# Kernel tuning notes

Hardware: AMD Instinct MI355X
Metric: run time of the kernel (lower is better)

The kernel has to match this reference:

```python
import jax, jax.numpy as jnp
import numpy as np

B, G, T, D = 512, 10, 100, 50
H, EMB, NEMB, OUT = 30, 20, 10, 10


def _gru_last_hidden(x, W_ih, W_hh, b_ih, b_hh):
    """PyTorch-convention GRU over x:[N,T,D]; returns final hidden [N,H].
    Gate order in the 3H dim is (r, z, n), matching torch.nn.GRU."""
    N = x.shape[0]
    # precompute input projections for all timesteps: [N,T,3H] -> [T,N,3H]
    xw = jnp.einsum('ntd,gd->ntg', x, W_ih) + b_ih
    xw = jnp.swapaxes(xw, 0, 1)
    h0 = jnp.zeros((N, H), dtype=x.dtype)

    def step(h, xw_t):
        gh = h @ W_hh.T + b_hh                      # [N,3H]
        r = jax.nn.sigmoid(xw_t[:, :H] + gh[:, :H])
        z = jax.nn.sigmoid(xw_t[:, H:2 * H] + gh[:, H:2 * H])
        n = jnp.tanh(xw_t[:, 2 * H:] + r * gh[:, 2 * H:])
        h = (1.0 - z) * n + z * h
        return h, None

    hT, _ = jax.lax.scan(step, h0, xw)
    return hT


def setup_inputs() -> dict:
    key = jax.random.key(0)
    ks = jax.random.split(key, 12)
    s_g = 1.0 / np.sqrt(H)
    inp = {
        'input1': jax.random.normal(ks[0], (B, G, T, D), jnp.float32),
        'input2': jax.random.normal(ks[1], (B, G, T, D), jnp.float32),
        'W_ih': jax.random.normal(ks[2], (3 * H, D), jnp.float32) * s_g,
        'W_hh': jax.random.normal(ks[3], (3 * H, H), jnp.float32) * s_g,
        'b_ih': jax.random.normal(ks[4], (3 * H,), jnp.float32) * s_g,
        'b_hh': jax.random.normal(ks[5], (3 * H,), jnp.float32) * s_g,
        'W1': jax.random.normal(ks[6], (EMB, H * G), jnp.float32) / np.sqrt(H * G),
        'b1': jax.random.normal(ks[7], (EMB,), jnp.float32) * 0.01,
        'W2': jax.random.normal(ks[8], (NEMB, EMB), jnp.float32) / np.sqrt(EMB),
        'b2': jax.random.normal(ks[9], (NEMB,), jnp.float32) * 0.01,
        'W3': jax.random.normal(ks[10], (OUT, NEMB), jnp.float32) / np.sqrt(NEMB),
        'b3': jax.random.normal(ks[11], (OUT,), jnp.float32) * 0.01,
    }
    return inp


def reference(input1, input2, W_ih, W_hh, b_ih, b_hh, W1, b1, W2, b2, W3, b3):
    gelu = lambda v: jax.nn.gelu(v, approximate=False)  # torch GELU default = exact
    # Fuse all num_gru slices of both inputs into one big batched GRU call
    x = jnp.concatenate([input1, input2], axis=0).reshape(2 * B * G, T, D)
    hT = _gru_last_hidden(x, W_ih, W_hh, b_ih, b_hh)    # [2BG, H]
    h = hT.reshape(2, B, G * H)                          # cat over num_gru == reshape
    embeddings1, embeddings2 = h[0], h[1]               # random_dis, MLP input
    logit_emb = gelu(embeddings2 @ W1.T + b1) @ W2.T + b2
    logit = gelu(logit_emb) @ W3.T + b3
    return logit, embeddings1
```

## Files before the change

### kernel.cpp

```cpp
#include <hip/hip_runtime.h>
#include <hip/hip_bf16.h>
#include <math.h>

#define T_    100
#define D_    50
#define H_    30
#define HALF  5120
#define EMB_  20
#define NEMB_ 10
#define OUT_  10

typedef _Float16 h2    __attribute__((ext_vector_type(2)));
typedef _Float16 f16x8 __attribute__((ext_vector_type(8)));
typedef float    f32x4 __attribute__((ext_vector_type(4)));

union FR  { f16x8 v; h2 p[4]; float4 f4; };

__device__ __forceinline__ h2 pk(float a, float b) {
    return __builtin_bit_cast(h2, __builtin_amdgcn_cvt_pkrtz(a, b));
}
__device__ __forceinline__ int pki(float a, float b) {
    return __builtin_bit_cast(int, __builtin_amdgcn_cvt_pkrtz(a, b));
}

#if __has_builtin(__builtin_amdgcn_exp2f)
#define EXP2(x) __builtin_amdgcn_exp2f(x)
#else
#define EXP2(x) exp2f(x)
#endif

struct XR { float2 a0, a1, a2, a3, b0, b1, b2, b3; };

__device__ __forceinline__ int rho(int j) {
    return (j & 3) + 4 * (j >> 3) + 16 * ((j >> 2) & 1);
}

__global__ __launch_bounds__(64, 1) void gru_kernel(
    const float* __restrict__ input1, const float* __restrict__ input2,
    const float* __restrict__ W_ih,  const float* __restrict__ W_hh,
    const float* __restrict__ b_ih,  const float* __restrict__ b_hh,
    float* __restrict__ emb1_out,
    float* __restrict__ h2_out)
{
    const int lane = threadIdx.x & 63;
    const int s    = lane & 15;
    const int q    = lane >> 4;
    const int n    = blockIdx.x * 16 + s;

    __shared__ __align__(16) _Float16 Wst [96 * 64];
    __shared__ __align__(16) _Float16 Whst[96 * 32];

    const float SC_RZ = -1.4426950408889634f;
    const float SC_N  =  2.8853900817779268f;

    for (int i = lane; i < 1536; i += 64) ((unsigned long long*)Wst)[i]  = 0ull;
    for (int i = lane; i < 768;  i += 64) ((unsigned long long*)Whst)[i] = 0ull;

    for (int i = 0; i < 71; ++i) {
        int idx = lane + i * 64;
        if (idx < 4500) {
            int rw = idx / 50, k = idx - rw * 50;
            int g  = rw / 30,  j = rw - g * 30;
            int ge = g * 32 + rho(j);
            float sc = (g < 2) ? SC_RZ : SC_N;
            Wst[ge * 64 + k] = (_Float16)(W_ih[idx] * sc);
        }
    }
    for (int i = 0; i < 2; ++i) {
        int idx = lane + i * 64;
        if (idx < 90) {
            int g = idx / 30, j = idx - g * 30;
            int ge = g * 32 + rho(j);
            float sc = (g < 2) ? SC_RZ : SC_N;
            Wst[ge * 64 + 50] = (_Float16)(b_ih[idx] * sc);
        }
    }
    for (int i = 0; i < 43; ++i) {
        int idx = lane + i * 64;
        if (idx < 2700) {
            int rw = idx / 30, k = idx - rw * 30;
            int g  = rw / 30,  j = rw - g * 30;
            int ge = g * 32 + rho(j);
            float sc = (g < 2) ? SC_RZ : SC_N;
            Whst[ge * 32 + k] = (_Float16)(W_hh[idx] * sc);
        }
    }
    for (int i = 0; i < 2; ++i) {
        int idx = lane + i * 64;
        if (idx < 90) {
            int g = idx / 30, j = idx - g * 30;
            int ge = g * 32 + rho(j);
            float sc = (g < 2) ? SC_RZ : SC_N;
            Whst[ge * 32 + 30] = (_Float16)(b_hh[idx] * sc);
        }
    }
    __syncthreads();

    FR wih[6][2], whh[6];
    #pragma unroll
    for (int nt = 0; nt < 6; ++nt) {
        wih[nt][0].f4 = *(const float4*)&Wst [(nt * 16 + s) * 64 + q * 8];
        wih[nt][1].f4 = *(const float4*)&Wst [(nt * 16 + s) * 64 + 32 + q * 8];
        whh[nt].f4    = *(const float4*)&Whst[(nt * 16 + s) * 32 + q * 8];
    }

    const float* xp = (n < HALF) ? input1 + (size_t)n * (T_ * D_)
                                 : input2 + (size_t)(n - HALF) * (T_ * D_);

    auto load_x = [&](int t, XR& X) {
        const float* r  = xp + t * D_;
        const float* pa = r + q * 8;
        const float* pb = (q < 2) ? (r + 32 + q * 8) : r;
        const float* p0 = (q == 2) ? (r + 48) : pb;
        X.a0 = *(const float2*)(pa + 0);
        X.a1 = *(const float2*)(pa + 2);
        X.a2 = *(const float2*)(pa + 4);
        X.a3 = *(const float2*)(pa + 6);
        X.b0 = *(const float2*)(p0);
        X.b1 = *(const float2*)(pb + 2);
        X.b2 = *(const float2*)(pb + 4);
        X.b3 = *(const float2*)(pb + 6);
    };
    auto build = [&](const XR& X, FR& x0, FR& x1) {
        x0.p[0] = pk(X.a0.x, X.a0.y); x0.p[1] = pk(X.a1.x, X.a1.y);
        x0.p[2] = pk(X.a2.x, X.a2.y); x0.p[3] = pk(X.a3.x, X.a3.y);
        if (q < 2) {
            x1.p[0] = pk(X.b0.x, X.b0.y); x1.p[1] = pk(X.b1.x, X.b1.y);
            x1.p[2] = pk(X.b2.x, X.b2.y); x1.p[3] = pk(X.b3.x, X.b3.y);
        } else if (q == 2) {
            x1.p[0] = pk(X.b0.x, X.b0.y); x1.p[1] = pk(1.f, 0.f);
            x1.p[2] = pk(0.f, 0.f);       x1.p[3] = pk(0.f, 0.f);
        } else {
            x1.p[0] = pk(0.f, 0.f); x1.p[1] = pk(0.f, 0.f);
            x1.p[2] = pk(0.f, 0.f); x1.p[3] = pk(0.f, 0.f);
        }
    };

    float hold[8] = {0.f, 0.f, 0.f, 0.f, 0.f, 0.f, 0.f, 0.f};
    int w0 = 0, w1 = 0, w2 = 0, w3 = 0;
    const int ONE = pki(1.f, 0.f);

    auto xphase = [&](XR& X, int tload, f32x4 (&xacc)[6]) {
        FR x0, x1;
        build(X, x0, x1);
        load_x(tload, X);
        #pragma unroll
        for (int i = 0; i < 6; ++i) {
            f32x4 zz = {0.f, 0.f, 0.f, 0.f};
            f32x4 a = __builtin_amdgcn_mfma_f32_16x16x32_f16(wih[i][0].v, x0.v, zz, 0, 0, 0);
            xacc[i] = __builtin_amdgcn_mfma_f32_16x16x32_f16(wih[i][1].v, x1.v, a, 0, 0, 0);
        }
    };
    auto step_h = [&](const f32x4 (&xacc)[6], f32x4 (&arz)[4], f32x4 (&ah)[2]) {
        FR bh;
        bh.p[0] = __builtin_bit_cast(h2, w0);
        bh.p[1] = __builtin_bit_cast(h2, w1);
        bh.p[2] = __builtin_bit_cast(h2, w2);
        bh.p[3] = __builtin_bit_cast(h2, q == 3 ? ONE : w3);
        #pragma unroll
        for (int nt = 0; nt < 4; ++nt)
            arz[nt] = __builtin_amdgcn_mfma_f32_16x16x32_f16(whh[nt].v, bh.v, xacc[nt], 0, 0, 0);
        #pragma unroll
        for (int u = 0; u < 2; ++u) {
            f32x4 zz = {0.f, 0.f, 0.f, 0.f};
            ah[u] = __builtin_amdgcn_mfma_f32_16x16x32_f16(whh[4 + u].v, bh.v, zz, 0, 0, 0);
        }
    };
    auto step_fin = [&](const f32x4 (&arz)[4], const f32x4 (&ah)[2],
                        const f32x4 (&xacc)[6]) {
        #pragma unroll
        for (int u = 0; u < 2; ++u) {
            #pragma unroll
            for (int r = 0; r < 4; ++r) {
                const float er = EXP2(arz[u][r]);
                const float rg = __builtin_amdgcn_rcpf(1.f + er);
                const float ez = EXP2(arz[2 + u][r]);
                const float aa = fmaf(rg, ah[u][r], xacc[4 + u][r]);
                const float et = EXP2(aa);
                const float oz = 1.f + ez, ot = 1.f + et;
                const float ip = __builtin_amdgcn_rcpf(oz * ot);
                const float zg = ot * ip;
                const float th = fmaf(-2.f * oz, ip, 1.f);
                hold[u * 4 + r] = fmaf(zg, hold[u * 4 + r] - th, th);
            }
        }
        w0 = pki(hold[0], hold[1]); w1 = pki(hold[2], hold[3]);
        w2 = pki(hold[4], hold[5]); w3 = pki(hold[6], hold[7]);
    };

    XR X0, X1, X2, X3;
    load_x(0, X0); load_x(1, X1); load_x(2, X2); load_x(3, X3);
    f32x4 xaccA[6], xaccB[6];
    {
        FR x0, x1;
        build(X0, x0, x1);
        load_x(4, X0);
        #pragma unroll
        for (int i = 0; i < 6; ++i) {
            f32x4 zz = {0.f, 0.f, 0.f, 0.f};
            f32x4 a = __builtin_amdgcn_mfma_f32_16x16x32_f16(wih[i][0].v, x0.v, zz, 0, 0, 0);
            xaccA[i] = __builtin_amdgcn_mfma_f32_16x16x32_f16(wih[i][1].v, x1.v, a, 0, 0, 0);
        }
    }

    #pragma unroll 1
    for (int k = 0; k < 25; ++k) {
        const int t = 4 * k;
        f32x4 arz[4], ah[2];
        step_h(xaccA, arz, ah);
        xphase(X1, (t + 5 < 100 ? t + 5 : 99), xaccB);
        step_fin(arz, ah, xaccA);
        step_h(xaccB, arz, ah);
        xphase(X2, (t + 6 < 100 ? t + 6 : 99), xaccA);
        step_fin(arz, ah, xaccB);
        step_h(xaccA, arz, ah);
        xphase(X3, (t + 7 < 100 ? t + 7 : 99), xaccB);
        step_fin(arz, ah, xaccA);
        step_h(xaccB, arz, ah);
        xphase(X0, (t + 8 < 100 ? t + 8 : 99), xaccA);
        step_fin(arz, ah, xaccB);
    }

    float* outp = (n < HALF) ? emb1_out + (size_t)n * H_
                             : h2_out + (size_t)(n - HALF) * H_;
    #pragma unroll
    for (int u = 0; u < 2; ++u)
        #pragma unroll
        for (int r = 0; r < 4; ++r) {
            const int j = 8 * q + 4 * u + r;
            if (j < H_) outp[j] = hold[u * 4 + r];
        }
}

__global__ __launch_bounds__(64) void mlp_kernel(
    const float* __restrict__ h2i,
    const float* __restrict__ W1, const float* __restrict__ b1,
    const float* __restrict__ W2, const float* __restrict__ b2,
    const float* __restrict__ W3, const float* __restrict__ b3,
    float* __restrict__ logit)
{
    const int b    = blockIdx.x;
    const int lane = threadIdx.x;
    __shared__ float e2[300];
    const float* row = h2i + (size_t)b * 300;
    #pragma unroll
    for (int i = lane; i < 75; i += 64)
        *(float4*)&e2[i * 4] = *(const float4*)(row + i * 4);
    __syncthreads();

    const float kInvSqrt2 = 0.70710678118654752f;
    float y1 = 0.f;
    if (lane < EMB_) {
        float acc = b1[lane];
        const float* wp = W1 + lane * 300;
        #pragma unroll
        for (int qq = 0; qq < 75; ++qq) {
            float4 wv = *(const float4*)(wp + qq * 4);
            acc += wv.x * e2[qq*4 + 0] + wv.y * e2[qq*4 + 1]
                 + wv.z * e2[qq*4 + 2] + wv.w * e2[qq*4 + 3];
        }
        y1 = 0.5f * acc * (1.f + erff(acc * kInvSqrt2));
    }
    float acc2 = (lane < NEMB_) ? b2[lane] : 0.f;
    #pragma unroll
    for (int e = 0; e < EMB_; ++e) {
        const float v = __shfl(y1, e);
        if (lane < NEMB_) acc2 += v * W2[lane * EMB_ + e];
    }
    const float y2 = 0.5f * acc2 * (1.f + erff(acc2 * kInvSqrt2));
    float acc3 = (lane < OUT_) ? b3[lane] : 0.f;
    #pragma unroll
    for (int e = 0; e < NEMB_; ++e) {
        const float v = __shfl(y2, e);
        if (lane < OUT_) acc3 += v * W3[lane * NEMB_ + e];
    }
    if (lane < OUT_) logit[(size_t)b * OUT_ + lane] = acc3;
}

extern "C" void kernel_launch(void* const* d_in, const int* in_sizes, int n_in,
                              void* d_out, int out_size, void* d_ws, size_t ws_size,
                              hipStream_t stream) {
    const float* input1 = (const float*)d_in[0];
    const float* input2 = (const float*)d_in[1];
    const float* W_ih   = (const float*)d_in[2];
    const float* W_hh   = (const float*)d_in[3];
    const float* b_ih   = (const float*)d_in[4];
    const float* b_hh   = (const float*)d_in[5];
    const float* W1     = (const float*)d_in[6];
    const float* b1     = (const float*)d_in[7];
    const float* W2     = (const float*)d_in[8];
    const float* b2     = (const float*)d_in[9];
    const float* W3     = (const float*)d_in[10];
    const float* b3     = (const float*)d_in[11];

    float* out = (float*)d_out;
    float* h2s = (float*)d_ws;

    hipLaunchKernelGGL(gru_kernel, dim3(640), dim3(64), 0, stream,
                       input1, input2, W_ih, W_hh, b_ih, b_hh,
                       out + 5120, h2s);
    hipLaunchKernelGGL(mlp_kernel, dim3(512), dim3(64), 0, stream,
                       h2s, W1, b1, W2, b2, W3, b3, out);
}
```

Measured before the change: 101.8 us.

## Stage GRU input chunks through double-buffered LDS with coalesced float4 loads

Replaces the per-lane strided float2 global loads of x with cooperative coalesced float4 loads of four-timestep chunks for all 16 sequences into a double-buffered shared-memory tile. Each step then reads its MFMA operands from LDS, and the next chunk's global load is issued one chunk ahead. The aim is better global coalescing and more latency hiding. In exchange it adds about 27KB of LDS and 13 float4 registers per lane, and there is no explicit barrier between the LDS write and the read. That is only safe because the block is a single wavefront.

```diff
diff --git a/kernel.cpp b/kernel.cpp
--- a/kernel.cpp
+++ b/kernel.cpp
@@ -49,6 +49,7 @@
 
     __shared__ __align__(16) _Float16 Wst [96 * 64];
     __shared__ __align__(16) _Float16 Whst[96 * 32];
+    __shared__ __align__(16) float    Xb[2][16 * 212];
 
     const float SC_RZ = -1.4426950408889634f;
     const float SC_N  =  2.8853900817779268f;
@@ -104,11 +105,34 @@
         whh[nt].f4    = *(const float4*)&Whst[(nt * 16 + s) * 32 + q * 8];
     }
 
-    const float* xp = (n < HALF) ? input1 + (size_t)n * (T_ * D_)
-                                 : input2 + (size_t)(n - HALF) * (T_ * D_);
-
-    auto load_x = [&](int t, XR& X) {
-        const float* r  = xp + t * D_;
+    const int n0 = blockIdx.x * 16;
+    const float* srcbase = (n0 < HALF) ? input1 + (size_t)n0 * (T_ * D_)
+                                       : input2 + (size_t)(n0 - HALF) * (T_ * D_);
+
+    int Poff[13], Wf[13];
+    #pragma unroll
+    for (int i = 0; i < 13; ++i) {
+        int g   = lane + i * 64;
+        int gg  = (g < 800) ? g : 0;
+        int sq  = gg / 50, rem = gg - sq * 50;
+        Poff[i] = sq * (T_ * D_) + rem * 4;
+        Wf[i]   = sq * 212 + rem * 4;
+    }
+    float4 G[13];
+    auto stage_load = [&](int cc) {
+        #pragma unroll
+        for (int i = 0; i < 13; ++i)
+            G[i] = *(const float4*)(srcbase + Poff[i] + cc * 200);
+    };
+    auto stage_write = [&](int nb) {
+        #pragma unroll
+        for (int i = 0; i < 13; ++i)
+            if (i < 12 || lane < 32)
+                *(float4*)&Xb[nb][Wf[i]] = G[i];
+    };
+
+    auto lds_read_x = [&](int buf, int tt, XR& X) {
+        const float* r  = &Xb[buf][s * 212 + tt * 50];
         const float* pa = r + q * 8;
         const float* pb = (q < 2) ? (r + 32 + q * 8) : r;
         const float* p0 = (q == 2) ? (r + 48) : pb;
@@ -140,10 +164,10 @@
     int w0 = 0, w1 = 0, w2 = 0, w3 = 0;
     const int ONE = pki(1.f, 0.f);
 
-    auto xphase = [&](XR& X, int tload, f32x4 (&xacc)[6]) {
-        FR x0, x1;
+    auto xphase = [&](int buf, int tt, f32x4 (&xacc)[6]) {
+        FR x0, x1; XR X;
+        lds_read_x(buf, tt, X);
         build(X, x0, x1);
-        load_x(tload, X);
         #pragma unroll
         for (int i = 0; i < 6; ++i) {
             f32x4 zz = {0.f, 0.f, 0.f, 0.f};
@@ -188,37 +212,22 @@
         w2 = pki(hold[4], hold[5]); w3 = pki(hold[6], hold[7]);
     };
 
-    XR X0, X1, X2, X3;
-    load_x(0, X0); load_x(1, X1); load_x(2, X2); load_x(3, X3);
+    stage_load(0);
+    stage_write(0);
+    stage_load(1);
     f32x4 xaccA[6], xaccB[6];
-    {
-        FR x0, x1;
-        build(X0, x0, x1);
-        load_x(4, X0);
-        #pragma unroll
-        for (int i = 0; i < 6; ++i) {
-            f32x4 zz = {0.f, 0.f, 0.f, 0.f};
-            f32x4 a = __builtin_amdgcn_mfma_f32_16x16x32_f16(wih[i][0].v, x0.v, zz, 0, 0, 0);
-            xaccA[i] = __builtin_amdgcn_mfma_f32_16x16x32_f16(wih[i][1].v, x1.v, a, 0, 0, 0);
-        }
-    }
+    xphase(0, 0, xaccA);
 
     #pragma unroll 1
-    for (int k = 0; k < 25; ++k) {
-        const int t = 4 * k;
+    for (int c = 0; c < 25; ++c) {
+        const int cur = c & 1, nxt = cur ^ 1;
+        stage_write(nxt);
+        stage_load(c + 2 > 24 ? 24 : c + 2);
         f32x4 arz[4], ah[2];
-        step_h(xaccA, arz, ah);
-        xphase(X1, (t + 5 < 100 ? t + 5 : 99), xaccB);
-        step_fin(arz, ah, xaccA);
-        step_h(xaccB, arz, ah);
-        xphase(X2, (t + 6 < 100 ? t + 6 : 99), xaccA);
-        step_fin(arz, ah, xaccB);
-        step_h(xaccA, arz, ah);
-        xphase(X3, (t + 7 < 100 ? t + 7 : 99), xaccB);
-        step_fin(arz, ah, xaccA);
-        step_h(xaccB, arz, ah);
-        xphase(X0, (t + 8 < 100 ? t + 8 : 99), xaccA);
-        step_fin(arz, ah, xaccB);
+        step_h(xaccA, arz, ah); xphase(cur, 1, xaccB); step_fin(arz, ah, xaccA);
+        step_h(xaccB, arz, ah); xphase(cur, 2, xaccA); step_fin(arz, ah, xaccB);
+        step_h(xaccA, arz, ah); xphase(cur, 3, xaccB); step_fin(arz, ah, xaccA);
+        step_h(xaccB, arz, ah); xphase(nxt, 0, xaccA); step_fin(arz, ah, xaccB);
     }
 
     float* outp = (n < HALF) ? emb1_out + (size_t)n * H_
```

After: 155.6 us. 1.53x slower.

## Split GRU hidden units across two wavefronts with LDS hidden-state exchange

Applied to the files above, without the earlier changes.

Each block now runs two wavefronts, and each wave owns half of the hidden units (one 16-row tile per gate). This halves the per-wave MFMA and transcendental work on the serial recurrence chain. The hidden state is exchanged through double-buffered shared memory with a barrier every timestep. In exchange it adds per-step LDS round trips and barrier latency on the critical path, while the x loads are duplicated in both waves.

```diff
diff --git a/kernel.cpp b/kernel.cpp
--- a/kernel.cpp
+++ b/kernel.cpp
@@ -35,29 +35,33 @@
     return (j & 3) + 4 * (j >> 3) + 16 * ((j >> 2) & 1);
 }
 
-__global__ __launch_bounds__(64, 1) void gru_kernel(
+__global__ __launch_bounds__(128, 1) void gru_kernel(
     const float* __restrict__ input1, const float* __restrict__ input2,
     const float* __restrict__ W_ih,  const float* __restrict__ W_hh,
     const float* __restrict__ b_ih,  const float* __restrict__ b_hh,
     float* __restrict__ emb1_out,
     float* __restrict__ h2_out)
 {
-    const int lane = threadIdx.x & 63;
+    const int tid  = threadIdx.x;
+    const int lane = tid & 63;
+    const int wv   = tid >> 6;
     const int s    = lane & 15;
     const int q    = lane >> 4;
     const int n    = blockIdx.x * 16 + s;
 
     __shared__ __align__(16) _Float16 Wst [96 * 64];
     __shared__ __align__(16) _Float16 Whst[96 * 32];
+    __shared__ __align__(8)  int2     Hx[2][2][64];
 
     const float SC_RZ = -1.4426950408889634f;
     const float SC_N  =  2.8853900817779268f;
 
-    for (int i = lane; i < 1536; i += 64) ((unsigned long long*)Wst)[i]  = 0ull;
-    for (int i = lane; i < 768;  i += 64) ((unsigned long long*)Whst)[i] = 0ull;
-
-    for (int i = 0; i < 71; ++i) {
-        int idx = lane + i * 64;
+    for (int i = tid; i < 1536; i += 128) ((unsigned long long*)Wst)[i]  = 0ull;
+    for (int i = tid; i < 768;  i += 128) ((unsigned long long*)Whst)[i] = 0ull;
+    __syncthreads();
+
+    for (int i = 0; i < 36; ++i) {
+        int idx = tid + i * 128;
         if (idx < 4500) {
             int rw = idx / 50, k = idx - rw * 50;
             int g  = rw / 30,  j = rw - g * 30;
@@ -66,17 +70,14 @@
             Wst[ge * 64 + k] = (_Float16)(W_ih[idx] * sc);
         }
     }
-    for (int i = 0; i < 2; ++i) {
-        int idx = lane + i * 64;
-        if (idx < 90) {
-            int g = idx / 30, j = idx - g * 30;
-            int ge = g * 32 + rho(j);
-            float sc = (g < 2) ? SC_RZ : SC_N;
-            Wst[ge * 64 + 50] = (_Float16)(b_ih[idx] * sc);
-        }
-    }
-    for (int i = 0; i < 43; ++i) {
-        int idx = lane + i * 64;
+    if (tid < 90) {
+        int g = tid / 30, j = tid - g * 30;
+        int ge = g * 32 + rho(j);
+        float sc = (g < 2) ? SC_RZ : SC_N;
+        Wst[ge * 64 + 50] = (_Float16)(b_ih[tid] * sc);
+    }
+    for (int i = 0; i < 22; ++i) {
+        int idx = tid + i * 128;
         if (idx < 2700) {
             int rw = idx / 30, k = idx - rw * 30;
             int g  = rw / 30,  j = rw - g * 30;
@@ -85,24 +86,25 @@
             Whst[ge * 32 + k] = (_Float16)(W_hh[idx] * sc);
         }
     }
-    for (int i = 0; i < 2; ++i) {
-        int idx = lane + i * 64;
-        if (idx < 90) {
-            int g = idx / 30, j = idx - g * 30;
-            int ge = g * 32 + rho(j);
-            float sc = (g < 2) ? SC_RZ : SC_N;
-            Whst[ge * 32 + 30] = (_Float16)(b_hh[idx] * sc);
-        }
+    if (tid < 90) {
+        int g = tid / 30, j = tid - g * 30;
+        int ge = g * 32 + rho(j);
+        float sc = (g < 2) ? SC_RZ : SC_N;
+        Whst[ge * 32 + 30] = (_Float16)(b_hh[tid] * sc);
     }
     __syncthreads();
 
-    FR wih[6][2], whh[6];
-    #pragma unroll
-    for (int nt = 0; nt < 6; ++nt) {
-        wih[nt][0].f4 = *(const float4*)&Wst [(nt * 16 + s) * 64 + q * 8];
-        wih[nt][1].f4 = *(const float4*)&Wst [(nt * 16 + s) * 64 + 32 + q * 8];
-        whh[nt].f4    = *(const float4*)&Whst[(nt * 16 + s) * 32 + q * 8];
-    }
+    const int tR = wv, tZ = 2 + wv, tN = 4 + wv;
+    FR wihR0, wihR1, wihZ0, wihZ1, wihN0, wihN1, whhR, whhZ, whhN;
+    wihR0.f4 = *(const float4*)&Wst [(tR * 16 + s) * 64 + q * 8];
+    wihR1.f4 = *(const float4*)&Wst [(tR * 16 + s) * 64 + 32 + q * 8];
+    wihZ0.f4 = *(const float4*)&Wst [(tZ * 16 + s) * 64 + q * 8];
+    wihZ1.f4 = *(const float4*)&Wst [(tZ * 16 + s) * 64 + 32 + q * 8];
+    wihN0.f4 = *(const float4*)&Wst [(tN * 16 + s) * 64 + q * 8];
+    wihN1.f4 = *(const float4*)&Wst [(tN * 16 + s) * 64 + 32 + q * 8];
+    whhR.f4  = *(const float4*)&Whst[(tR * 16 + s) * 32 + q * 8];
+    whhZ.f4  = *(const float4*)&Whst[(tZ * 16 + s) * 32 + q * 8];
+    whhN.f4  = *(const float4*)&Whst[(tN * 16 + s) * 32 + q * 8];
 
     const float* xp = (n < HALF) ? input1 + (size_t)n * (T_ * D_)
                                  : input2 + (size_t)(n - HALF) * (T_ * D_);
@@ -136,100 +138,112 @@
         }
     };
 
-    float hold[8] = {0.f, 0.f, 0.f, 0.f, 0.f, 0.f, 0.f, 0.f};
-    int w0 = 0, w1 = 0, w2 = 0, w3 = 0;
-    const int ONE = pki(1.f, 0.f);
-
-    auto xphase = [&](XR& X, int tload, f32x4 (&xacc)[6]) {
+    float hold[4] = {0.f, 0.f, 0.f, 0.f};
+    int2 mine   = {0, 0};
+    int2 theirs = {0, 0};
+    const int ONE  = pki(1.f, 0.f);
+    const int hidx = s * 4 + q;
+
+    auto xphase = [&](XR& X, int tload, f32x4 (&xacc)[3]) {
         FR x0, x1;
         build(X, x0, x1);
         load_x(tload, X);
+        f32x4 zz = {0.f, 0.f, 0.f, 0.f};
+        f32x4 a;
+        a = __builtin_amdgcn_mfma_f32_16x16x32_f16(wihR0.v, x0.v, zz, 0, 0, 0);
+        xacc[0] = __builtin_amdgcn_mfma_f32_16x16x32_f16(wihR1.v, x1.v, a, 0, 0, 0);
+        a = __builtin_amdgcn_mfma_f32_16x16x32_f16(wihZ0.v, x0.v, zz, 0, 0, 0);
+        xacc[1] = __builtin_amdgcn_mfma_f32_16x16x32_f16(wihZ1.v, x1.v, a, 0, 0, 0);
+        a = __builtin_amdgcn_mfma_f32_16x16x32_f16(wihN0.v, x0.v, zz, 0, 0, 0);
+        xacc[2] = __builtin_amdgcn_mfma_f32_16x16x32_f16(wihN1.v, x1.v, a, 0, 0, 0);
+    };
+    auto step_h = [&](const f32x4 (&xacc)[3], f32x4& ar, f32x4& az, f32x4& anh) {
+        const int p0 = wv ? theirs.x : mine.x;
+        const int p1 = wv ? theirs.y : mine.y;
+        const int p2 = wv ? mine.x   : theirs.x;
+        const int p3 = wv ? mine.y   : theirs.y;
+        FR bh;
+        bh.p[0] = __builtin_bit_cast(h2, p0);
+        bh.p[1] = __builtin_bit_cast(h2, p1);
+        bh.p[2] = __builtin_bit_cast(h2, p2);
+        bh.p[3] = __builtin_bit_cast(h2, q == 3 ? ONE : p3);
+        f32x4 zz = {0.f, 0.f, 0.f, 0.f};
+        ar  = __builtin_amdgcn_mfma_f32_16x16x32_f16(whhR.v, bh.v, xacc[0], 0, 0, 0);
+        az  = __builtin_amdgcn_mfma_f32_16x16x32_f16(whhZ.v, bh.v, xacc[1], 0, 0, 0);
+        anh = __builtin_amdgcn_mfma_f32_16x16x32_f16(whhN.v, bh.v, zz,      0, 0, 0);
+    };
+    auto step_fin = [&](const f32x4& ar, const f32x4& az, const f32x4& anh,
+                        const f32x4& anx) {
         #pragma unroll
-        for (int i = 0; i < 6; ++i) {
-            f32x4 zz = {0.f, 0.f, 0.f, 0.f};
-            f32x4 a = __builtin_amdgcn_mfma_f32_16x16x32_f16(wih[i][0].v, x0.v, zz, 0, 0, 0);
-            xacc[i] = __builtin_amdgcn_mfma_f32_16x16x32_f16(wih[i][1].v, x1.v, a, 0, 0, 0);
-        }
-    };
-    auto step_h = [&](const f32x4 (&xacc)[6], f32x4 (&arz)[4], f32x4 (&ah)[2]) {
-        FR bh;
-        bh.p[0] = __builtin_bit_cast(h2, w0);
-        bh.p[1] = __builtin_bit_cast(h2, w1);
-        bh.p[2] = __builtin_bit_cast(h2, w2);
-        bh.p[3] = __builtin_bit_cast(h2, q == 3 ? ONE : w3);
-        #pragma unroll
-        for (int nt = 0; nt < 4; ++nt)
-            arz[nt] = __builtin_amdgcn_mfma_f32_16x16x32_f16(whh[nt].v, bh.v, xacc[nt], 0, 0, 0);
-        #pragma unroll
-        for (int u = 0; u < 2; ++u) {
-            f32x4 zz = {0.f, 0.f, 0.f, 0.f};
-            ah[u] = __builtin_amdgcn_mfma_f32_16x16x32_f16(whh[4 + u].v, bh.v, zz, 0, 0, 0);
-        }
-    };
-    auto step_fin = [&](const f32x4 (&arz)[4], const f32x4 (&ah)[2],
-                        const f32x4 (&xacc)[6]) {
-        #pragma unroll
-        for (int u = 0; u < 2; ++u) {
-            #pragma unroll
-            for (int r = 0; r < 4; ++r) {
-                const float er = EXP2(arz[u][r]);
-                const float rg = __builtin_amdgcn_rcpf(1.f + er);
-                const float ez = EXP2(arz[2 + u][r]);
-                const float aa = fmaf(rg, ah[u][r], xacc[4 + u][r]);
-                const float et = EXP2(aa);
-                const float oz = 1.f + ez, ot = 1.f + et;
-                const float ip = __builtin_amdgcn_rcpf(oz * ot);
-                const float zg = ot * ip;
-                const float th = fmaf(-2.f * oz, ip, 1.f);
-                hold[u * 4 + r] = fmaf(zg, hold[u * 4 + r] - th, th);
-            }
-        }
-        w0 = pki(hold[0], hold[1]); w1 = pki(hold[2], hold[3]);
-        w2 = pki(hold[4], hold[5]); w3 = pki(hold[6], hold[7]);
+        for (int r = 0; r < 4; ++r) {
+            const float er = EXP2(ar[r]);
+            const float rg = __builtin_amdgcn_rcpf(1.f + er);
+            const float ez = EXP2(az[r]);
+            const float aa = fmaf(rg, anh[r], anx[r]);
+            const float et = EXP2(aa);
+            const float oz = 1.f + ez, ot = 1.f + et;
+            const float ip = __builtin_amdgcn_rcpf(oz * ot);
+            const float zg = ot * ip;
+            const float th = fmaf(-2.f * oz, ip, 1.f);
+            hold[r] = fmaf(zg, hold[r] - th, th);
+        }
+        mine.x = pki(hold[0], hold[1]);
+        mine.y = pki(hold[2], hold[3]);
+    };
+    auto exchange = [&](int par) {
+        Hx[par][wv][hidx] = mine;
+        asm volatile("s_waitcnt lgkmcnt(0)" ::: "memory");
+        __builtin_amdgcn_s_barrier();
+        __builtin_amdgcn_sched_barrier(0);
+        theirs = Hx[par][wv ^ 1][hidx];
     };
 
     XR X0, X1, X2, X3;
     load_x(0, X0); load_x(1, X1); load_x(2, X2); load_x(3, X3);
-    f32x4 xaccA[6], xaccB[6];
+    f32x4 xaccA[3], xaccB[3];
     {
         FR x0, x1;
         build(X0, x0, x1);
         load_x(4, X0);
-        #pragma unroll
-        for (int i = 0; i < 6; ++i) {
-            f32x4 zz = {0.f, 0.f, 0.f, 0.f};
-            f32x4 a = __builtin_amdgcn_mfma_f32_16x16x32_f16(wih[i][0].v, x0.v, zz, 0, 0, 0);
-            xaccA[i] = __builtin_amdgcn_mfma_f32_16x16x32_f16(wih[i][1].v, x1.v, a, 0, 0, 0);
-        }
+        f32x4 zz = {0.f, 0.f, 0.f, 0.f};
+        f32x4 a;
+        a = __builtin_amdgcn_mfma_f32_16x16x32_f16(wihR0.v, x0.v, zz, 0, 0, 0);
+        xaccA[0] = __builtin_amdgcn_mfma_f32_16x16x32_f16(wihR1.v, x1.v, a, 0, 0, 0);
+        a = __builtin_amdgcn_mfma_f32_16x16x32_f16(wihZ0.v, x0.v, zz, 0, 0, 0);
+        xaccA[1] = __builtin_amdgcn_mfma_f32_16x16x32_f16(wihZ1.v, x1.v, a, 0, 0, 0);
+        a = __builtin_amdgcn_mfma_f32_16x16x32_f16(wihN0.v, x0.v, zz, 0, 0, 0);
+        xaccA[2] = __builtin_amdgcn_mfma_f32_16x16x32_f16(wihN1.v, x1.v, a, 0, 0, 0);
     }
 
     #pragma unroll 1
     for (int k = 0; k < 25; ++k) {
         const int t = 4 * k;
-        f32x4 arz[4], ah[2];
-        step_h(xaccA, arz, ah);
+        f32x4 ar, az, anh;
+        step_h(xaccA, ar, az, anh);
         xphase(X1, (t + 5 < 100 ? t + 5 : 99), xaccB);
-        step_fin(arz, ah, xaccA);
-        step_h(xaccB, arz, ah);
+        step_fin(ar, az, anh, xaccA[2]);
+        exchange(0);
+        step_h(xaccB, ar, az, anh);
         xphase(X2, (t + 6 < 100 ? t + 6 : 99), xaccA);
-        step_fin(arz, ah, xaccB);
-        step_h(xaccA, arz, ah);
+        step_fin(ar, az, anh, xaccB[2]);
+        exchange(1);
+        step_h(xaccA, ar, az, anh);
         xphase(X3, (t + 7 < 100 ? t + 7 : 99), xaccB);
-        step_fin(arz, ah, xaccA);
-        step_h(xaccB, arz, ah);
+        step_fin(ar, az, anh, xaccA[2]);
+        exchange(0);
+        step_h(xaccB, ar, az, anh);
         xphase(X0, (t + 8 < 100 ? t + 8 : 99), xaccA);
-        step_fin(arz, ah, xaccB);
+        step_fin(ar, az, anh, xaccB[2]);
+        exchange(1);
     }
 
     float* outp = (n < HALF) ? emb1_out + (size_t)n * H_
                              : h2_out + (size_t)(n - HALF) * H_;
     #pragma unroll
-    for (int u = 0; u < 2; ++u)
-        #pragma unroll
-        for (int r = 0; r < 4; ++r) {
-            const int j = 8 * q + 4 * u + r;
-            if (j < H_) outp[j] = hold[u * 4 + r];
-        }
+    for (int r = 0; r < 4; ++r) {
+        const int j = 8 * q + 4 * wv + r;
+        if (j < H_) outp[j] = hold[r];
+    }
 }
 
 __global__ __launch_bounds__(64) void mlp_kernel(
@@ -296,7 +310,7 @@
     float* out = (float*)d_out;
     float* h2s = (float*)d_ws;
 
-    hipLaunchKernelGGL(gru_kernel, dim3(640), dim3(64), 0, stream,
+    hipLaunchKernelGGL(gru_kernel, dim3(640), dim3(128), 0, stream,
                        input1, input2, W_ih, W_hh, b_ih, b_hh,
                        out + 5120, h2s);
     hipLaunchKernelGGL(mlp_kernel, dim3(512), dim3(64), 0, stream,
```

Result: faster. 96.79 us (median of 3 runs) (-5.0%).
